# Optimization experiments

Measured on AMD Instinct MI355X. Metric: run time of the kernel, lower is better.

Reference implementation:

```python
import jax, jax.numpy as jnp
import numpy as np

B, L, C = 2, 512, 64
EPS = 1e-5

def layer_norm(x, w, b):
    mu = jnp.mean(x, axis=-1, keepdims=True)
    var = jnp.mean(jnp.square(x - mu), axis=-1, keepdims=True)
    return (x - mu) * jax.lax.rsqrt(var + EPS) * w + b

def setup_inputs() -> dict:
    key = jax.random.key(0)
    ks = jax.random.split(key, 16)
    s = 1.0 / np.sqrt(C)
    def lin(k):
        k1, k2 = jax.random.split(k)
        return (jax.random.uniform(k1, (C, C), jnp.float32, -s, s),
                jax.random.uniform(k2, (C,), jnp.float32, -s, s))
    W_lp, b_lp = lin(ks[0]); W_rp, b_rp = lin(ks[1])
    W_lg, b_lg = lin(ks[2]); W_rg, b_rg = lin(ks[3])
    W_og, b_og = lin(ks[4]); W_out, b_out = lin(ks[5])
    return {
        'pairwise_states': jax.random.normal(ks[6], (B, L, L, C), jnp.float32),
        'attention_mask': jnp.ones((B, 1, 1, L), jnp.float32),
        'ln_in_w': jnp.ones((C,), jnp.float32), 'ln_in_b': jnp.zeros((C,), jnp.float32),
        'W_lp': W_lp, 'b_lp': b_lp, 'W_rp': W_rp, 'b_rp': b_rp,
        'W_lg': W_lg, 'b_lg': b_lg, 'W_rg': W_rg, 'b_rg': b_rg,
        'W_og': W_og, 'b_og': b_og,
        'ln_out_w': jnp.ones((C,), jnp.float32), 'ln_out_b': jnp.zeros((C,), jnp.float32),
        'W_out': W_out, 'b_out': b_out,
    }

def reference(pairwise_states, attention_mask, ln_in_w, ln_in_b,
              W_lp, b_lp, W_rp, b_rp, W_lg, b_lg, W_rg, b_rg,
              W_og, b_og, ln_out_w, ln_out_b, W_out, b_out):
    residual = pairwise_states
    x = layer_norm(pairwise_states, ln_in_w, ln_in_b)  # [B,L,L,C]
    left = x @ W_lp + b_lp
    right = x @ W_rp + b_rp
    # attention_mask [B,1,1,L].transpose(1,3) -> [B,L,1,1]: masks the i (row) axis
    m = jnp.transpose(attention_mask, (0, 3, 2, 1))
    left = left * m
    right = right * m
    left = left * jax.nn.sigmoid(x @ W_lg + b_lg)
    right = right * jax.nn.sigmoid(x @ W_rg + b_rg)
    out_gate = jax.nn.sigmoid(x @ W_og + b_og)
    # outgoing triangle update: out[b,i,j,c] = sum_k left[b,i,k,c] * right[b,j,k,c]
    tri = jnp.einsum('bikc,bjkc->bijc', left, right)
    y = layer_norm(tri, ln_out_w, ln_out_b) * out_gate
    y = y @ W_out + b_out
    return y + residual
```

## Files before the change

kernel.cpp:

```cpp
#include <hip/hip_runtime.h>
#include <cstdint>

typedef float f32x4 __attribute__((ext_vector_type(4)));
typedef short s16x8 __attribute__((ext_vector_type(8)));

#define APAD 72

__device__ __forceinline__ unsigned short f2bf(float f) {
  union { float f; uint32_t u; } v; v.f = f;
  uint32_t u = v.u;
  u += 0x7fffu + ((u >> 16) & 1u);
  return (unsigned short)(u >> 16);
}
__device__ __forceinline__ float bf2f(unsigned short h) {
  union { uint32_t u; float f; } v; v.u = ((uint32_t)h) << 16;
  return v.f;
}
__device__ __forceinline__ uint32_t pkbf(float a, float b) {
  uint32_t r;
  asm("v_cvt_pk_bf16_f32 %0, %1, %2" : "=v"(r) : "v"(a), "v"(b));
  return r;
}
__device__ __forceinline__ float sigmoidf_(float x) {
  return 1.0f / (1.0f + __expf(-x));
}
__device__ __forceinline__ f32x4 zero4() {
  f32x4 z = {0.f, 0.f, 0.f, 0.f};
  return z;
}
__device__ __forceinline__ void gl_lds16(const void* g, void* l) {
  __builtin_amdgcn_global_load_lds(
      (const __attribute__((address_space(1))) uint32_t*)g,
      (__attribute__((address_space(3))) uint32_t*)l, 16, 0, 0);
}

__global__ __launch_bounds__(256) void k_prep(
    const float* __restrict__ Wlp, const float* __restrict__ Wrp,
    const float* __restrict__ Wlg, const float* __restrict__ Wrg,
    const float* __restrict__ Wog, const float* __restrict__ Wout,
    unsigned short* __restrict__ wt) {
  const float* srcs[6] = {Wlp, Wrp, Wlg, Wrg, Wog, Wout};
  const int m = blockIdx.x;
  const float* W = srcs[m];
  const int t = threadIdx.x;
  for (int e = t; e < 64 * APAD; e += 256) {
    const int n = e / APAD, k = e - n * APAD;
    wt[m * (64 * APAD) + e] = (k < 64) ? f2bf(W[k * 64 + n]) : (unsigned short)0;
  }
}

__global__ __launch_bounds__(256, 4) void k1_proj(
    const float* __restrict__ xin, const float* __restrict__ mask,
    const float* __restrict__ lnw, const float* __restrict__ lnb,
    const float* __restrict__ blp, const float* __restrict__ brp,
    const float* __restrict__ blg, const float* __restrict__ brg,
    const unsigned short* __restrict__ wt,
    unsigned short* __restrict__ leftT, unsigned short* __restrict__ rightT) {
  __shared__ unsigned short A[64 * APAD];
  __shared__ unsigned short TL[64 * APAD];
  __shared__ unsigned short TR[64 * APAD];
  const int tid = threadIdx.x, lane = tid & 63, w = tid >> 6;
  const int bid = blockIdx.x;
  const int b = bid >> 12;
  const int i = (bid >> 3) & 511;
  const int k0 = (bid & 7) << 6;

  const int pair = w >> 1, ch = w & 1;
  const int kh8 = (lane >> 4) << 3;
  s16x8 wp[2][2], wg[2][2];
  float bPv[2], bGv[2];
  {
    const unsigned short* wtP = wt + (size_t)pair * (64 * APAD);
    const unsigned short* wtG = wt + (size_t)(2 + pair) * (64 * APAD);
    const float* bP = pair ? brp : blp;
    const float* bG = pair ? brg : blg;
#pragma unroll
    for (int nf2 = 0; nf2 < 2; ++nf2) {
      const int n = ch * 32 + nf2 * 16 + (lane & 15);
      const unsigned short* pp = wtP + n * APAD + kh8;
      const unsigned short* pg = wtG + n * APAD + kh8;
      wp[nf2][0] = *(const s16x8*)pp;  wp[nf2][1] = *(const s16x8*)(pp + 32);
      wg[nf2][0] = *(const s16x8*)pg;  wg[nf2][1] = *(const s16x8*)(pg + 32);
      bPv[nf2] = bP[n];  bGv[nf2] = bG[n];
    }
  }

  const int p = tid >> 2, q = tid & 3;
  const float* xrow = xin + (((size_t)b * 512 + i) * 512 + k0 + p) * 64 + q * 16;
  f32x4 xv[4];
#pragma unroll
  for (int u = 0; u < 4; ++u) xv[u] = ((const f32x4*)xrow)[u];
  float s1 = 0.f, s2 = 0.f;
#pragma unroll
  for (int u = 0; u < 4; ++u)
#pragma unroll
    for (int e = 0; e < 4; ++e) { float t = xv[u][e]; s1 += t; s2 += t * t; }
  s1 += __shfl_xor(s1, 1); s2 += __shfl_xor(s2, 1);
  s1 += __shfl_xor(s1, 2); s2 += __shfl_xor(s2, 2);
  const float mu = s1 * 0.015625f;
  const float rs = rsqrtf(s2 * 0.015625f - mu * mu + 1e-5f);
  {
    uint32_t pk[8];
#pragma unroll
    for (int u = 0; u < 4; ++u) {
      f32x4 wv = ((const f32x4*)(lnw + q * 16))[u];
      f32x4 bv = ((const f32x4*)(lnb + q * 16))[u];
#pragma unroll
      for (int e2 = 0; e2 < 2; ++e2) {
        pk[u * 2 + e2] = pkbf((xv[u][2 * e2] - mu) * rs * wv[2 * e2] + bv[2 * e2],
                              (xv[u][2 * e2 + 1] - mu) * rs * wv[2 * e2 + 1] + bv[2 * e2 + 1]);
      }
    }
    uint32_t* a32 = (uint32_t*)&A[p * APAD + q * 16];
#pragma unroll
    for (int u = 0; u < 8; ++u) a32[u] = pk[u];
  }
  const float mval = mask[b * 512 + i];
  __syncthreads();

  const int fr4 = (lane >> 4) << 2;
  unsigned short* T = pair ? TR : TL;
#pragma unroll
  for (int mf = 0; mf < 4; ++mf) {
    const int ar = (mf * 16 + (lane & 15)) * APAD + kh8;
    const s16x8 a0 = *(const s16x8*)&A[ar];
    const s16x8 a1 = *(const s16x8*)&A[ar + 32];
    f32x4 accP[2], accG[2];
#pragma unroll
    for (int nf2 = 0; nf2 < 2; ++nf2) {
      accP[nf2] = zero4(); accG[nf2] = zero4();
      accP[nf2] = __builtin_amdgcn_mfma_f32_16x16x32_bf16(a0, wp[nf2][0], accP[nf2], 0, 0, 0);
      accP[nf2] = __builtin_amdgcn_mfma_f32_16x16x32_bf16(a1, wp[nf2][1], accP[nf2], 0, 0, 0);
      accG[nf2] = __builtin_amdgcn_mfma_f32_16x16x32_bf16(a0, wg[nf2][0], accG[nf2], 0, 0, 0);
      accG[nf2] = __builtin_amdgcn_mfma_f32_16x16x32_bf16(a1, wg[nf2][1], accG[nf2], 0, 0, 0);
    }
    const int prow = mf * 16 + fr4;
#pragma unroll
    for (int nf2 = 0; nf2 < 2; ++nf2) {
      const int n = ch * 32 + nf2 * 16 + (lane & 15);
      const float bl = bPv[nf2], bg = bGv[nf2];
      float v0 = (accP[nf2][0] + bl) * mval * sigmoidf_(accG[nf2][0] + bg);
      float v1 = (accP[nf2][1] + bl) * mval * sigmoidf_(accG[nf2][1] + bg);
      float v2 = (accP[nf2][2] + bl) * mval * sigmoidf_(accG[nf2][2] + bg);
      float v3 = (accP[nf2][3] + bl) * mval * sigmoidf_(accG[nf2][3] + bg);
      *(uint32_t*)&T[n * APAD + prow] = pkbf(v0, v1);
      *(uint32_t*)&T[n * APAD + prow + 2] = pkbf(v2, v3);
    }
  }
  __syncthreads();

  {
    const int sn = tid >> 2, sq = tid & 3;
    const size_t gbase = (((size_t)b * 64 + sn) * 512 + i) * 512 + k0 + sq * 16;
    const uint32_t* sl = (const uint32_t*)&TL[sn * APAD + sq * 16];
    const uint32_t* sr = (const uint32_t*)&TR[sn * APAD + sq * 16];
    uint32_t* dl = (uint32_t*)(leftT + gbase);
    uint32_t* dr = (uint32_t*)(rightT + gbase);
#pragma unroll
    for (int u = 0; u < 8; ++u) dl[u] = sl[u];
#pragma unroll
    for (int u = 0; u < 8; ++u) dr[u] = sr[u];
  }
}

__global__ __launch_bounds__(256) void k2_gemm(
    const unsigned short* __restrict__ leftT,
    const unsigned short* __restrict__ rightT,
    unsigned short* __restrict__ triT) {
  __shared__ unsigned short Ab[2][128 * 64];
  __shared__ unsigned short Bb[2][128 * 64];
  const int tid = threadIdx.x, lane = tid & 63, w = tid >> 6;
  const int bid = blockIdx.x;
  const int sw = ((bid & 7) << 8) | (bid >> 3);
  const int plane = sw >> 4, tile = sw & 15;
  const size_t pb = (size_t)plane * 262144;
  const int i0 = (tile >> 2) << 7, j0 = (tile & 3) << 7;
  const int srow = lane >> 3;
  const int sk = (((lane & 7) ^ (lane >> 3)) << 3);

  f32x4 acc[4][4];
#pragma unroll
  for (int mf = 0; mf < 4; ++mf)
#pragma unroll
    for (int nf = 0; nf < 4; ++nf) acc[mf][nf] = zero4();
  const int wr = (w >> 1) << 6, wc = (w & 1) << 6;

  auto stage = [&](int buf, int kt) {
    const int kk = kt << 6;
#pragma unroll
    for (int it = 0; it < 4; ++it) {
      const int ch = it * 4 + w;
      const int row = (ch << 3) + srow;
      gl_lds16(leftT + pb + (size_t)(i0 + row) * 512 + kk + sk,
               (char*)&Ab[buf][0] + ch * 1024 + lane * 16);
      gl_lds16(rightT + pb + (size_t)(j0 + row) * 512 + kk + sk,
               (char*)&Bb[buf][0] + ch * 1024 + lane * 16);
    }
  };

  stage(0, 0);
  for (int kt = 0; kt < 8; ++kt) {
    __syncthreads();
    if (kt < 7) stage((kt & 1) ^ 1, kt + 1);
    const unsigned short* Ac = &Ab[kt & 1][0];
    const unsigned short* Bc = &Bb[kt & 1][0];
#pragma unroll
    for (int ks = 0; ks < 2; ++ks) {
      const int ko = ((lane >> 4) << 3) + (ks << 5);
      const int kosw = ko ^ ((lane & 7) << 3);
      s16x8 af[4], bfr[4];
#pragma unroll
      for (int mf = 0; mf < 4; ++mf)
        af[mf] = *(const s16x8*)&Ac[(wr + mf * 16 + (lane & 15)) * 64 + kosw];
#pragma unroll
      for (int nf = 0; nf < 4; ++nf)
        bfr[nf] = *(const s16x8*)&Bc[(wc + nf * 16 + (lane & 15)) * 64 + kosw];
#pragma unroll
      for (int mf = 0; mf < 4; ++mf)
#pragma unroll
        for (int nf = 0; nf < 4; ++nf)
          acc[mf][nf] = __builtin_amdgcn_mfma_f32_16x16x32_bf16(af[mf], bfr[nf], acc[mf][nf], 0, 0, 0);
    }
  }
  __syncthreads();
  unsigned short* Tt = &Ab[0][0];
#pragma unroll
  for (int mf = 0; mf < 4; ++mf)
#pragma unroll
    for (int nf = 0; nf < 4; ++nf) {
      const int col = wc + nf * 16 + (lane & 15);
#pragma unroll
      for (int r = 0; r < 4; ++r) {
        const int row = wr + mf * 16 + ((lane >> 4) << 2) + r;
        Tt[row * 128 + col] = f2bf(acc[mf][nf][r]);
      }
    }
  __syncthreads();
  {
    const int row = tid >> 1, half = (tid & 1) << 6;
    const uint32_t* src = (const uint32_t*)&Tt[row * 128 + half];
    uint32_t* dst = (uint32_t*)(triT + pb + (size_t)(i0 + row) * 512 + j0 + half);
#pragma unroll
    for (int u = 0; u < 32; ++u) dst[u] = src[u];
  }
}

#define OPAD 68
__global__ __launch_bounds__(256, 4) void k3_out(
    const unsigned short* __restrict__ triT,
    const float* __restrict__ resid,
    const float* __restrict__ lnw1, const float* __restrict__ lnb1,
    const float* __restrict__ bog,
    const float* __restrict__ lnw2, const float* __restrict__ lnb2,
    const float* __restrict__ bout,
    const unsigned short* __restrict__ wt,
    float* __restrict__ outp) {
  __shared__ __align__(16) unsigned char smem[36864];
  unsigned short* WT = (unsigned short*)smem;
  unsigned short* Y  = (unsigned short*)(smem + 9216);
  unsigned short* X  = (unsigned short*)(smem + 18432);
  unsigned short* OG = (unsigned short*)(smem + 27648);
  float* OUT32 = (float*)(smem + 18432);
  const int tid = threadIdx.x, lane = tid & 63, w = tid >> 6;
  const int bid = blockIdx.x;
  const int b = bid >> 12;
  const int i = (bid >> 3) & 511;
  const int j0 = (bid & 7) << 6;

  {
    const char* wsrc = (const char*)(wt + (size_t)4 * (64 * APAD));
#pragma unroll
    for (int it = 0; it < 3; ++it) {
      const int off = (it * 256 + tid) * 16;
      if (off < 9216) gl_lds16(wsrc + off, (char*)WT + off);
    }
  }

  const int j = tid >> 2, q = tid & 3;
  {
    const int c = tid >> 2;
    const int csw = c ^ (q << 4);
    const size_t srow = ((size_t)(b * 64 + c) * 512 + i) * 512 + j0 + q * 16;
    union { uint32_t u32[8]; unsigned short s[16]; } uu;
    const uint32_t* s32 = (const uint32_t*)(triT + srow);
#pragma unroll
    for (int u = 0; u < 8; ++u) uu.u32[u] = s32[u];
#pragma unroll
    for (int s = 0; s < 16; ++s) Y[(q * 16 + s) * APAD + csw] = uu.s[s];
  }
  f32x4 rv[4];
  {
    const float* rrow = resid + (((size_t)b * 512 + i) * 512 + j0 + j) * 64 + q * 16;
#pragma unroll
    for (int u = 0; u < 4; ++u) rv[u] = ((const f32x4*)rrow)[u];
    float s1 = 0.f, s2 = 0.f;
#pragma unroll
    for (int u = 0; u < 4; ++u)
#pragma unroll
      for (int e = 0; e < 4; ++e) { float t = rv[u][e]; s1 += t; s2 += t * t; }
    s1 += __shfl_xor(s1, 1); s2 += __shfl_xor(s2, 1);
    s1 += __shfl_xor(s1, 2); s2 += __shfl_xor(s2, 2);
    const float mu = s1 * 0.015625f;
    const float rs = rsqrtf(s2 * 0.015625f - mu * mu + 1e-5f);
    uint32_t pk[8];
#pragma unroll
    for (int u = 0; u < 4; ++u) {
      f32x4 wv = ((const f32x4*)(lnw1 + q * 16))[u];
      f32x4 bv = ((const f32x4*)(lnb1 + q * 16))[u];
#pragma unroll
      for (int e2 = 0; e2 < 2; ++e2) {
        pk[u * 2 + e2] = pkbf((rv[u][2 * e2] - mu) * rs * wv[2 * e2] + bv[2 * e2],
                              (rv[u][2 * e2 + 1] - mu) * rs * wv[2 * e2 + 1] + bv[2 * e2 + 1]);
      }
    }
    uint32_t* x32 = (uint32_t*)&X[j * APAD + q * 16];
#pragma unroll
    for (int u = 0; u < 8; ++u) x32[u] = pk[u];
  }
  __syncthreads();

  const int qx = q ^ (w & 3);
  float yv[16];
  {
    union { uint32_t u32[8]; unsigned short s[16]; } uy;
    const uint32_t* y32 = (const uint32_t*)&Y[j * APAD + (qx << 4)];
#pragma unroll
    for (int u = 0; u < 8; ++u) uy.u32[u] = y32[u];
#pragma unroll
    for (int s = 0; s < 16; ++s) yv[s] = bf2f(uy.s[s]);
  }
  float t1 = 0.f, t2 = 0.f;
#pragma unroll
  for (int s = 0; s < 16; ++s) { t1 += yv[s]; t2 += yv[s] * yv[s]; }
  t1 += __shfl_xor(t1, 1); t2 += __shfl_xor(t2, 1);
  t1 += __shfl_xor(t1, 2); t2 += __shfl_xor(t2, 2);
  const float mu2 = t1 * 0.015625f;
  const float rs2 = rsqrtf(t2 * 0.015625f - mu2 * mu2 + 1e-5f);

  const int kh8 = (lane >> 4) << 3;
  {
    const int xrow = (w * 16 + (lane & 15)) * APAD;
    const s16x8 xb0 = *(const s16x8*)&X[xrow + kh8];
    const s16x8 xb1 = *(const s16x8*)&X[xrow + kh8 + 32];
    const int jcol = w * 16 + (lane & 15);
    uint32_t* og32 = (uint32_t*)&OG[jcol * APAD];
#pragma unroll
    for (int nf = 0; nf < 4; ++nf) {
      const int wrow = (nf * 16 + (lane & 15)) * APAD;
      const s16x8 wa0 = *(const s16x8*)&WT[wrow + kh8];
      const s16x8 wa1 = *(const s16x8*)&WT[wrow + kh8 + 32];
      f32x4 aog = zero4();
      aog = __builtin_amdgcn_mfma_f32_16x16x32_bf16(wa0, xb0, aog, 0, 0, 0);
      aog = __builtin_amdgcn_mfma_f32_16x16x32_bf16(wa1, xb1, aog, 0, 0, 0);
      const f32x4 bb4 = ((const f32x4*)bog)[(lane >> 4) + 4 * nf];
      const float s0 = sigmoidf_(aog[0] + bb4[0]);
      const float s1_ = sigmoidf_(aog[1] + bb4[1]);
      const float s2_ = sigmoidf_(aog[2] + bb4[2]);
      const float s3 = sigmoidf_(aog[3] + bb4[3]);
      const int c2 = (lane >> 4) * 2 + nf * 8;
      og32[c2] = pkbf(s0, s1_);
      og32[c2 + 1] = pkbf(s2_, s3);
    }
  }
  __syncthreads();

  {
    const char* wsrc2 = (const char*)(wt + (size_t)5 * (64 * APAD));
#pragma unroll
    for (int it = 0; it < 3; ++it) {
      const int off = (it * 256 + tid) * 16;
      if (off < 9216) gl_lds16(wsrc2 + off, (char*)WT + off);
    }
  }

  {
    union { uint32_t u32[8]; unsigned short s[16]; } og_;
    const uint32_t* o32 = (const uint32_t*)&OG[j * APAD + q * 16];
#pragma unroll
    for (int u = 0; u < 8; ++u) og_.u32[u] = o32[u];
    uint32_t pk[8];
#pragma unroll
    for (int u = 0; u < 4; ++u) {
      f32x4 wv = ((const f32x4*)(lnw2 + q * 16))[u];
      f32x4 bv = ((const f32x4*)(lnb2 + q * 16))[u];
#pragma unroll
      for (int e2 = 0; e2 < 2; ++e2) {
        const int s0 = u * 4 + 2 * e2;
        float y0 = ((yv[s0] - mu2) * rs2 * wv[2 * e2] + bv[2 * e2]) * bf2f(og_.s[s0]);
        float y1 = ((yv[s0 + 1] - mu2) * rs2 * wv[2 * e2 + 1] + bv[2 * e2 + 1]) * bf2f(og_.s[s0 + 1]);
        pk[u * 2 + e2] = pkbf(y0, y1);
      }
    }
    uint32_t* y32 = (uint32_t*)&Y[j * APAD + (qx << 4)];
#pragma unroll
    for (int u = 0; u < 8; ++u) y32[u] = pk[u];
  }
  __syncthreads();

  {
    const int xsw = (w & 3) << 4;
    const int arow = (w * 16 + (lane & 15)) * APAD;
    const s16x8 a0 = *(const s16x8*)&Y[arow + (kh8 ^ xsw)];
    const s16x8 a1 = *(const s16x8*)&Y[arow + ((32 + kh8) ^ xsw)];
    f32x4 ao[4];
#pragma unroll
    for (int nf = 0; nf < 4; ++nf) ao[nf] = zero4();
#pragma unroll
    for (int nf = 0; nf < 4; ++nf) {
      const int brow = (nf * 16 + (lane & 15)) * APAD + kh8;
      const s16x8 b0 = *(const s16x8*)&WT[brow];
      const s16x8 b1 = *(const s16x8*)&WT[brow + 32];
      ao[nf] = __builtin_amdgcn_mfma_f32_16x16x32_bf16(a0, b0, ao[nf], 0, 0, 0);
      ao[nf] = __builtin_amdgcn_mfma_f32_16x16x32_bf16(a1, b1, ao[nf], 0, 0, 0);
    }
#pragma unroll
    for (int nf = 0; nf < 4; ++nf) {
      const int n = nf * 16 + (lane & 15);
      const float bo = bout[n];
#pragma unroll
      for (int r = 0; r < 4; ++r) {
        const int prow = w * 16 + ((lane >> 4) << 2) + r;
        OUT32[prow * OPAD + n] = ao[nf][r] + bo;
      }
    }
  }
  __syncthreads();

  {
    const size_t gb = (((size_t)b * 512 + i) * 512 + j0 + j) * 64 + q * 16;
    float* op = outp + gb;
#pragma unroll
    for (int u = 0; u < 4; ++u) {
      f32x4 ov = ((const f32x4*)&OUT32[j * OPAD + q * 16])[u];
      ((f32x4*)op)[u] = ov + rv[u];
    }
  }
}

extern "C" void kernel_launch(void* const* d_in, const int* in_sizes, int n_in,
                              void* d_out, int out_size, void* d_ws, size_t ws_size,
                              hipStream_t stream) {
  const float* x     = (const float*)d_in[0];
  const float* mask  = (const float*)d_in[1];
  const float* lnw1  = (const float*)d_in[2];
  const float* lnb1  = (const float*)d_in[3];
  const float* Wlp   = (const float*)d_in[4];
  const float* blp   = (const float*)d_in[5];
  const float* Wrp   = (const float*)d_in[6];
  const float* brp   = (const float*)d_in[7];
  const float* Wlg   = (const float*)d_in[8];
  const float* blg   = (const float*)d_in[9];
  const float* Wrg   = (const float*)d_in[10];
  const float* brg   = (const float*)d_in[11];
  const float* Wog   = (const float*)d_in[12];
  const float* bog   = (const float*)d_in[13];
  const float* lnw2  = (const float*)d_in[14];
  const float* lnb2  = (const float*)d_in[15];
  const float* Wout  = (const float*)d_in[16];
  const float* bout  = (const float*)d_in[17];

  unsigned short* leftT  = (unsigned short*)d_ws;
  unsigned short* rightT = leftT + (size_t)33554432;
  unsigned short* triT   = rightT + (size_t)33554432;
  unsigned short* wt     = triT + (size_t)33554432;

  k_prep<<<6, 256, 0, stream>>>(Wlp, Wrp, Wlg, Wrg, Wog, Wout, wt);
  k1_proj<<<8192, 256, 0, stream>>>(x, mask, lnw1, lnb1, blp, brp, blg, brg,
                                    wt, leftT, rightT);
  k2_gemm<<<2048, 256, 0, stream>>>(leftT, rightT, triT);
  k3_out<<<8192, 256, 0, stream>>>(triT, x, lnw1, lnb1, bog, lnw2, lnb2, bout,
                                   wt, (float*)d_out);
}
```

Before: 249.5 us.

## Halve GEMM k-tile for occupancy; keep out-gate in registers in output kernel

In the triangle GEMM kernel the k-tile shrinks from 64 to 32, so shared memory drops to 32 KB and the launch bounds ask for 4 blocks per CU, with the swizzle and k-loop count adjusted to match. In the output kernel both weight matrices are preloaded into shared memory at the start, and the second LayerNorm is computed in MFMA-fragment layout. This lets the sigmoid gate values stay in registers and removes the OG shared-memory buffer, one barrier and the mid-kernel weight reload. The cost is twice as many k-iterations and barriers in the GEMM, and a possibly higher register count.

```diff
diff --git a/kernel.cpp b/kernel.cpp
--- a/kernel.cpp
+++ b/kernel.cpp
@@ -163,20 +163,19 @@
   }
 }
 
-__global__ __launch_bounds__(256) void k2_gemm(
+__global__ __launch_bounds__(256, 4) void k2_gemm(
     const unsigned short* __restrict__ leftT,
     const unsigned short* __restrict__ rightT,
     unsigned short* __restrict__ triT) {
-  __shared__ unsigned short Ab[2][128 * 64];
-  __shared__ unsigned short Bb[2][128 * 64];
+  __shared__ __align__(16) unsigned short S[4 * 4096];
   const int tid = threadIdx.x, lane = tid & 63, w = tid >> 6;
   const int bid = blockIdx.x;
   const int sw = ((bid & 7) << 8) | (bid >> 3);
   const int plane = sw >> 4, tile = sw & 15;
   const size_t pb = (size_t)plane * 262144;
   const int i0 = (tile >> 2) << 7, j0 = (tile & 3) << 7;
-  const int srow = lane >> 3;
-  const int sk = (((lane & 7) ^ (lane >> 3)) << 3);
+  const int srow = lane >> 2;
+  const int sk = (((lane & 3) ^ ((lane >> 2) & 3)) << 3);
 
   f32x4 acc[4][4];
 #pragma unroll
@@ -186,49 +185,46 @@
   const int wr = (w >> 1) << 6, wc = (w & 1) << 6;
 
   auto stage = [&](int buf, int kt) {
-    const int kk = kt << 6;
-#pragma unroll
-    for (int it = 0; it < 4; ++it) {
+    const int kk = kt << 5;
+#pragma unroll
+    for (int it = 0; it < 2; ++it) {
       const int ch = it * 4 + w;
-      const int row = (ch << 3) + srow;
+      const int row = (ch << 4) + srow;
       gl_lds16(leftT + pb + (size_t)(i0 + row) * 512 + kk + sk,
-               (char*)&Ab[buf][0] + ch * 1024 + lane * 16);
+               (char*)S + buf * 16384 + ch * 1024 + lane * 16);
       gl_lds16(rightT + pb + (size_t)(j0 + row) * 512 + kk + sk,
-               (char*)&Bb[buf][0] + ch * 1024 + lane * 16);
+               (char*)S + buf * 16384 + 8192 + ch * 1024 + lane * 16);
     }
   };
 
   stage(0, 0);
-  for (int kt = 0; kt < 8; ++kt) {
+  const int l15 = lane & 15;
+  const int kosw = ((lane >> 4) ^ (lane & 3)) << 3;
+  for (int kt = 0; kt < 16; ++kt) {
     __syncthreads();
-    if (kt < 7) stage((kt & 1) ^ 1, kt + 1);
-    const unsigned short* Ac = &Ab[kt & 1][0];
-    const unsigned short* Bc = &Bb[kt & 1][0];
-#pragma unroll
-    for (int ks = 0; ks < 2; ++ks) {
-      const int ko = ((lane >> 4) << 3) + (ks << 5);
-      const int kosw = ko ^ ((lane & 7) << 3);
-      s16x8 af[4], bfr[4];
-#pragma unroll
-      for (int mf = 0; mf < 4; ++mf)
-        af[mf] = *(const s16x8*)&Ac[(wr + mf * 16 + (lane & 15)) * 64 + kosw];
+    if (kt < 15) stage((kt & 1) ^ 1, kt + 1);
+    const unsigned short* Ac = S + (kt & 1) * 8192;
+    const unsigned short* Bc = Ac + 4096;
+    s16x8 af[4], bfr[4];
+#pragma unroll
+    for (int mf = 0; mf < 4; ++mf)
+      af[mf] = *(const s16x8*)&Ac[(wr + mf * 16 + l15) * 32 + kosw];
+#pragma unroll
+    for (int nf = 0; nf < 4; ++nf)
+      bfr[nf] = *(const s16x8*)&Bc[(wc + nf * 16 + l15) * 32 + kosw];
+#pragma unroll
+    for (int mf = 0; mf < 4; ++mf)
 #pragma unroll
       for (int nf = 0; nf < 4; ++nf)
-        bfr[nf] = *(const s16x8*)&Bc[(wc + nf * 16 + (lane & 15)) * 64 + kosw];
-#pragma unroll
-      for (int mf = 0; mf < 4; ++mf)
-#pragma unroll
-        for (int nf = 0; nf < 4; ++nf)
-          acc[mf][nf] = __builtin_amdgcn_mfma_f32_16x16x32_bf16(af[mf], bfr[nf], acc[mf][nf], 0, 0, 0);
-    }
-  }
-  __syncthreads();
-  unsigned short* Tt = &Ab[0][0];
+        acc[mf][nf] = __builtin_amdgcn_mfma_f32_16x16x32_bf16(af[mf], bfr[nf], acc[mf][nf], 0, 0, 0);
+  }
+  __syncthreads();
+  unsigned short* Tt = S;
 #pragma unroll
   for (int mf = 0; mf < 4; ++mf)
 #pragma unroll
     for (int nf = 0; nf < 4; ++nf) {
-      const int col = wc + nf * 16 + (lane & 15);
+      const int col = wc + nf * 16 + l15;
 #pragma unroll
       for (int r = 0; r < 4; ++r) {
         const int row = wr + mf * 16 + ((lane >> 4) << 2) + r;
@@ -256,10 +252,10 @@
     const unsigned short* __restrict__ wt,
     float* __restrict__ outp) {
   __shared__ __align__(16) unsigned char smem[36864];
-  unsigned short* WT = (unsigned short*)smem;
-  unsigned short* Y  = (unsigned short*)(smem + 9216);
-  unsigned short* X  = (unsigned short*)(smem + 18432);
-  unsigned short* OG = (unsigned short*)(smem + 27648);
+  unsigned short* WTog  = (unsigned short*)smem;
+  unsigned short* WTout = (unsigned short*)(smem + 9216);
+  unsigned short* Y     = (unsigned short*)(smem + 18432);
+  unsigned short* X     = (unsigned short*)(smem + 27648);
   float* OUT32 = (float*)(smem + 18432);
   const int tid = threadIdx.x, lane = tid & 63, w = tid >> 6;
   const int bid = blockIdx.x;
@@ -270,9 +266,9 @@
   {
     const char* wsrc = (const char*)(wt + (size_t)4 * (64 * APAD));
 #pragma unroll
-    for (int it = 0; it < 3; ++it) {
+    for (int it = 0; it < 5; ++it) {
       const int off = (it * 256 + tid) * 16;
-      if (off < 9216) gl_lds16(wsrc + off, (char*)WT + off);
+      if (off < 18432) gl_lds16(wsrc + off, (char*)WTog + off);
     }
   }
 
@@ -319,107 +315,89 @@
   }
   __syncthreads();
 
-  const int qx = q ^ (w & 3);
+  const int l15 = lane & 15, hi = lane >> 4;
+  const int jrow = w * 16 + l15;
+  const int ybase = jrow * APAD;
+  const int kh8 = hi << 3;
   float yv[16];
-  {
-    union { uint32_t u32[8]; unsigned short s[16]; } uy;
-    const uint32_t* y32 = (const uint32_t*)&Y[j * APAD + (qx << 4)];
-#pragma unroll
-    for (int u = 0; u < 8; ++u) uy.u32[u] = y32[u];
-#pragma unroll
-    for (int s = 0; s < 16; ++s) yv[s] = bf2f(uy.s[s]);
+#pragma unroll
+  for (int nf = 0; nf < 4; ++nf) {
+    const int pc = (((nf ^ w) & 3) << 4) + (hi << 2);
+    const uint2 dd = *(const uint2*)&Y[ybase + pc];
+    yv[nf * 4 + 0] = bf2f((unsigned short)(dd.x & 0xffff));
+    yv[nf * 4 + 1] = bf2f((unsigned short)(dd.x >> 16));
+    yv[nf * 4 + 2] = bf2f((unsigned short)(dd.y & 0xffff));
+    yv[nf * 4 + 3] = bf2f((unsigned short)(dd.y >> 16));
   }
   float t1 = 0.f, t2 = 0.f;
 #pragma unroll
   for (int s = 0; s < 16; ++s) { t1 += yv[s]; t2 += yv[s] * yv[s]; }
-  t1 += __shfl_xor(t1, 1); t2 += __shfl_xor(t2, 1);
-  t1 += __shfl_xor(t1, 2); t2 += __shfl_xor(t2, 2);
+  t1 += __shfl_xor(t1, 16); t2 += __shfl_xor(t2, 16);
+  t1 += __shfl_xor(t1, 32); t2 += __shfl_xor(t2, 32);
   const float mu2 = t1 * 0.015625f;
   const float rs2 = rsqrtf(t2 * 0.015625f - mu2 * mu2 + 1e-5f);
 
-  const int kh8 = (lane >> 4) << 3;
-  {
-    const int xrow = (w * 16 + (lane & 15)) * APAD;
-    const s16x8 xb0 = *(const s16x8*)&X[xrow + kh8];
-    const s16x8 xb1 = *(const s16x8*)&X[xrow + kh8 + 32];
-    const int jcol = w * 16 + (lane & 15);
-    uint32_t* og32 = (uint32_t*)&OG[jcol * APAD];
+  float sg[16];
+  {
+    const s16x8 xb0 = *(const s16x8*)&X[ybase + kh8];
+    const s16x8 xb1 = *(const s16x8*)&X[ybase + kh8 + 32];
 #pragma unroll
     for (int nf = 0; nf < 4; ++nf) {
-      const int wrow = (nf * 16 + (lane & 15)) * APAD;
-      const s16x8 wa0 = *(const s16x8*)&WT[wrow + kh8];
-      const s16x8 wa1 = *(const s16x8*)&WT[wrow + kh8 + 32];
+      const int wrow = (nf * 16 + l15) * APAD + kh8;
+      const s16x8 wa0 = *(const s16x8*)&WTog[wrow];
+      const s16x8 wa1 = *(const s16x8*)&WTog[wrow + 32];
       f32x4 aog = zero4();
       aog = __builtin_amdgcn_mfma_f32_16x16x32_bf16(wa0, xb0, aog, 0, 0, 0);
       aog = __builtin_amdgcn_mfma_f32_16x16x32_bf16(wa1, xb1, aog, 0, 0, 0);
-      const f32x4 bb4 = ((const f32x4*)bog)[(lane >> 4) + 4 * nf];
-      const float s0 = sigmoidf_(aog[0] + bb4[0]);
-      const float s1_ = sigmoidf_(aog[1] + bb4[1]);
-      const float s2_ = sigmoidf_(aog[2] + bb4[2]);
-      const float s3 = sigmoidf_(aog[3] + bb4[3]);
-      const int c2 = (lane >> 4) * 2 + nf * 8;
-      og32[c2] = pkbf(s0, s1_);
-      og32[c2 + 1] = pkbf(s2_, s3);
-    }
-  }
-  __syncthreads();
-
-  {
-    const char* wsrc2 = (const char*)(wt + (size_t)5 * (64 * APAD));
-#pragma unroll
-    for (int it = 0; it < 3; ++it) {
-      const int off = (it * 256 + tid) * 16;
-      if (off < 9216) gl_lds16(wsrc2 + off, (char*)WT + off);
-    }
-  }
-
-  {
-    union { uint32_t u32[8]; unsigned short s[16]; } og_;
-    const uint32_t* o32 = (const uint32_t*)&OG[j * APAD + q * 16];
-#pragma unroll
-    for (int u = 0; u < 8; ++u) og_.u32[u] = o32[u];
-    uint32_t pk[8];
-#pragma unroll
-    for (int u = 0; u < 4; ++u) {
-      f32x4 wv = ((const f32x4*)(lnw2 + q * 16))[u];
-      f32x4 bv = ((const f32x4*)(lnb2 + q * 16))[u];
-#pragma unroll
-      for (int e2 = 0; e2 < 2; ++e2) {
-        const int s0 = u * 4 + 2 * e2;
-        float y0 = ((yv[s0] - mu2) * rs2 * wv[2 * e2] + bv[2 * e2]) * bf2f(og_.s[s0]);
-        float y1 = ((yv[s0 + 1] - mu2) * rs2 * wv[2 * e2 + 1] + bv[2 * e2 + 1]) * bf2f(og_.s[s0 + 1]);
-        pk[u * 2 + e2] = pkbf(y0, y1);
-      }
-    }
-    uint32_t* y32 = (uint32_t*)&Y[j * APAD + (qx << 4)];
-#pragma unroll
-    for (int u = 0; u < 8; ++u) y32[u] = pk[u];
+      const f32x4 bb4 = *(const f32x4*)(bog + nf * 16 + (hi << 2));
+      sg[nf * 4 + 0] = sigmoidf_(aog[0] + bb4[0]);
+      sg[nf * 4 + 1] = sigmoidf_(aog[1] + bb4[1]);
+      sg[nf * 4 + 2] = sigmoidf_(aog[2] + bb4[2]);
+      sg[nf * 4 + 3] = sigmoidf_(aog[3] + bb4[3]);
+    }
+  }
+#pragma unroll
+  for (int nf = 0; nf < 4; ++nf) {
+    const f32x4 wv = *(const f32x4*)(lnw2 + nf * 16 + (hi << 2));
+    const f32x4 bv = *(const f32x4*)(lnb2 + nf * 16 + (hi << 2));
+    const float y0 = ((yv[nf * 4 + 0] - mu2) * rs2 * wv[0] + bv[0]) * sg[nf * 4 + 0];
+    const float y1 = ((yv[nf * 4 + 1] - mu2) * rs2 * wv[1] + bv[1]) * sg[nf * 4 + 1];
+    const float y2 = ((yv[nf * 4 + 2] - mu2) * rs2 * wv[2] + bv[2]) * sg[nf * 4 + 2];
+    const float y3 = ((yv[nf * 4 + 3] - mu2) * rs2 * wv[3] + bv[3]) * sg[nf * 4 + 3];
+    uint2 o;
+    o.x = pkbf(y0, y1);
+    o.y = pkbf(y2, y3);
+    const int pc = (((nf ^ w) & 3) << 4) + (hi << 2);
+    *(uint2*)&Y[ybase + pc] = o;
   }
   __syncthreads();
 
   {
     const int xsw = (w & 3) << 4;
-    const int arow = (w * 16 + (lane & 15)) * APAD;
-    const s16x8 a0 = *(const s16x8*)&Y[arow + (kh8 ^ xsw)];
-    const s16x8 a1 = *(const s16x8*)&Y[arow + ((32 + kh8) ^ xsw)];
+    const s16x8 a0 = *(const s16x8*)&Y[ybase + (kh8 ^ xsw)];
+    const s16x8 a1 = *(const s16x8*)&Y[ybase + ((32 + kh8) ^ xsw)];
+    s16x8 wb0[4], wb1[4];
+#pragma unroll
+    for (int nf = 0; nf < 4; ++nf) {
+      const int brow = (nf * 16 + l15) * APAD + kh8;
+      wb0[nf] = *(const s16x8*)&WTout[brow];
+      wb1[nf] = *(const s16x8*)&WTout[brow + 32];
+    }
+    __syncthreads();
     f32x4 ao[4];
 #pragma unroll
-    for (int nf = 0; nf < 4; ++nf) ao[nf] = zero4();
-#pragma unroll
     for (int nf = 0; nf < 4; ++nf) {
-      const int brow = (nf * 16 + (lane & 15)) * APAD + kh8;
-      const s16x8 b0 = *(const s16x8*)&WT[brow];
-      const s16x8 b1 = *(const s16x8*)&WT[brow + 32];
-      ao[nf] = __builtin_amdgcn_mfma_f32_16x16x32_bf16(a0, b0, ao[nf], 0, 0, 0);
-      ao[nf] = __builtin_amdgcn_mfma_f32_16x16x32_bf16(a1, b1, ao[nf], 0, 0, 0);
+      ao[nf] = zero4();
+      ao[nf] = __builtin_amdgcn_mfma_f32_16x16x32_bf16(a0, wb0[nf], ao[nf], 0, 0, 0);
+      ao[nf] = __builtin_amdgcn_mfma_f32_16x16x32_bf16(a1, wb1[nf], ao[nf], 0, 0, 0);
     }
 #pragma unroll
     for (int nf = 0; nf < 4; ++nf) {
-      const int n = nf * 16 + (lane & 15);
+      const int n = nf * 16 + l15;
       const float bo = bout[n];
 #pragma unroll
       for (int r = 0; r < 4; ++r) {
-        const int prow = w * 16 + ((lane >> 4) << 2) + r;
+        const int prow = w * 16 + (hi << 2) + r;
         OUT32[prow * OPAD + n] = ao[nf][r] + bo;
       }
     }
```

Result: faster. 242.5 us (-2.8%).
